# Performance work log

Hardware: AMD Instinct MI355X
Metric: run time of the kernel (lower is better)

The kernel has to match this reference:

```python
import jax, jax.numpy as jnp
import numpy as np

B, S, H, K = 8, 2048, 768, 128
FILTERS = (1, 3, 5)
C = H // len(FILTERS)  # 256 channels per conv, concat -> H
LN_EPS = 1e-05
COS_EPS = 1e-08


def setup_inputs() -> dict:
    key = jax.random.key(0)
    ks = jax.random.split(key, 16)
    mk = lambda k, shape: jax.random.normal(k, shape, dtype=jnp.float32) * 0.02
    return {
        "representation": jax.random.normal(ks[0], (B, S, H), dtype=jnp.float32),
        "src_mask": jnp.ones((B, S), dtype=jnp.float32),
        # conv weights stored as [k, H_in, C_out] for lax 1D conv (torch Conv2d(1,C,(k,H)))
        "enc_conv_w1": mk(ks[1], (1, H, C)),
        "enc_conv_w3": mk(ks[2], (3, H, C)),
        "enc_conv_w5": mk(ks[3], (5, H, C)),
        "ln_g": jnp.ones((H,), jnp.float32),
        "ln_b": jnp.zeros((H,), jnp.float32),
        "enc_lin_w": mk(ks[4], (H, H)),   # torch Linear weight [out,in]
        "enc_tr_w": mk(ks[5], (K, H)),
        "dec_tr_w": mk(ks[6], (H, K)),
        "dec_conv_w1": mk(ks[7], (1, H, C)),
        "dec_conv_w3": mk(ks[8], (3, H, C)),
        "dec_conv_w5": mk(ks[9], (5, H, C)),
        "dec_lin_w": mk(ks[10], (H, H)),
        "out_lin_w": mk(ks[11], (H, H)),
    }


def _multi_conv(x, ws):
    # x: [B, S, H]; each w: [k, H, C]; torch pads (k//2, 0) -> same-length for odd k
    outs = []
    for w in ws:
        k = w.shape[0]
        outs.append(jax.lax.conv_general_dilated(
            x, w, window_strides=(1,), padding=[(k // 2, k // 2)],
            dimension_numbers=("NWC", "WIO", "NWC")))
    return jnp.concatenate(outs, axis=-1)  # [B, S, H]


def _layernorm(x, g, b):
    mu = jnp.mean(x, axis=-1, keepdims=True)
    var = jnp.mean((x - mu) ** 2, axis=-1, keepdims=True)
    return (x - mu) * jax.lax.rsqrt(var + LN_EPS) * g + b


def reference(representation, src_mask, enc_conv_w1, enc_conv_w3, enc_conv_w5,
              ln_g, ln_b, enc_lin_w, enc_tr_w, dec_tr_w,
              dec_conv_w1, dec_conv_w3, dec_conv_w5, dec_lin_w, out_lin_w):
    # ---- AutoEncoder (dropout layers are identity in eval mode) ----
    h = _multi_conv(representation, (enc_conv_w1, enc_conv_w3, enc_conv_w5))
    h = _layernorm(h + representation, ln_g, ln_b)
    h = jnp.tanh(h @ enc_lin_w.T)
    location = h @ enc_tr_w.T            # [B, S, K] (encode_out)
    d = location @ dec_tr_w.T            # [B, S, H]
    d = _multi_conv(d, (dec_conv_w1, dec_conv_w3, dec_conv_w5))
    d = jnp.tanh(d @ dec_lin_w.T)
    decode_out = d @ out_lin_w.T         # [B, S, H]

    # ---- banded pairwise cosine similarity (fuses the torch shift loop) ----
    # torch loop writes dis_matrix[b, i, i+s+1] = cos(loc[b, i+s+1], loc[b, i])
    # for s in range(max_act_len), i.e. the strict upper band of the symmetric
    # pairwise cosine-similarity matrix with offsets 1..max_act_len.
    normed = location / jnp.maximum(
        jnp.sqrt(jnp.sum(location * location, axis=-1, keepdims=True)), COS_EPS)
    sim = jnp.einsum("bid,bjd->bij", normed, normed)  # [B, S, S]
    offs = jnp.arange(S)[None, :] - jnp.arange(S)[:, None]  # j - i
    max_act_len = jnp.max(jnp.sum(src_mask, axis=-1)).astype(jnp.int32)
    band = (offs >= 1) & (offs <= max_act_len)        # [S, S]
    dis_matrix = jnp.where(band[None], sim, 0.0)
    src_dis_mask = src_mask[:, :, None] * src_mask[:, None, :]
    act_dis_tags = band[None].astype(jnp.float32) * src_dis_mask
    return (location, dis_matrix, act_dis_tags, decode_out)
```

## Files before the change

### kernel.cpp

```cpp
#include <hip/hip_runtime.h>

#define B_   8
#define S_   2048
#define H_   768
#define K_   128
#define C_   256
#define SH_  2052
#define MTOK (B_*S_)

typedef __attribute__((ext_vector_type(8))) short short8;
typedef __attribute__((ext_vector_type(4))) float f32x4;

typedef __attribute__((address_space(1))) const void gvoid;
typedef __attribute__((address_space(3))) void lvoid;

__device__ __forceinline__ void gload16(const void* g, void* l) {
    __builtin_amdgcn_global_load_lds((gvoid*)g, (lvoid*)l, 16, 0, 0);
}

__device__ __forceinline__ ushort f2b(float f) {
    union { float f; unsigned u; } v; v.f = f;
    unsigned r = v.u + 0x7fffu + ((v.u >> 16) & 1u);
    return (ushort)(r >> 16);
}
__device__ __forceinline__ float b2f(ushort u) {
    union { unsigned u; float f; } v; v.u = ((unsigned)u) << 16;
    return v.f;
}
__device__ __forceinline__ float fast_tanh(float x) {
    float e = __expf(2.f * x);
    return 1.f - 2.f / (e + 1.f);
}


__global__ __launch_bounds__(512) void k_maxlen(const float* __restrict__ mask, int* Lp) {
    __shared__ float sh[8];
    const int tid = threadIdx.x;
    float mx = 0.f;
    for (int b = 0; b < B_; ++b) {
        const float4 v = ((const float4*)(mask + b * S_))[tid];
        float s = v.x + v.y + v.z + v.w;
#pragma unroll
        for (int off = 32; off; off >>= 1) s += __shfl_xor(s, off);
        if ((tid & 63) == 0) sh[tid >> 6] = s;
        __syncthreads();
        if (tid == 0) {
            float t = 0.f;
#pragma unroll
            for (int q = 0; q < 8; ++q) t += sh[q];
            mx = fmaxf(mx, t);
        }
        __syncthreads();
    }
    if (tid == 0) *Lp = (int)mx;
}

__global__ void k_build_xh(const float* __restrict__ rep, ushort* __restrict__ xh) {
    int i = blockIdx.x * blockDim.x + threadIdx.x;
    const int stride = gridDim.x * blockDim.x;
    const int n4 = B_ * SH_ * H_ / 4;
    for (; i < n4; i += stride) {
        const int idx = i * 4;
        const int h = idx % H_;
        const int rs = idx / H_;
        const int s = rs % SH_;
        const int b = rs / SH_;
        ushort4 o; o.x = 0; o.y = 0; o.z = 0; o.w = 0;
        if (s >= 2 && s < S_ + 2) {
            const float4 v = *(const float4*)(rep + ((size_t)b * S_ + (s - 2)) * H_ + h);
            o.x = f2b(v.x); o.y = f2b(v.y); o.z = f2b(v.z); o.w = f2b(v.w);
        }
        *(ushort4*)(xh + idx) = o;
    }
}

struct CvtE { const float* src; ushort* dst; int n; int kh; };
struct CvtAll { CvtE e[11]; };

__global__ void k_cvt_all(CvtAll a) {
    const CvtE e = a.e[blockIdx.y];
    int i = blockIdx.x * blockDim.x + threadIdx.x;
    const int stride = gridDim.x * blockDim.x;
    for (; i < e.n; i += stride) {
        if (e.kh) {
            const int c = i / e.kh;
            const int r = i - c * e.kh;
            e.dst[i] = f2b(e.src[r * C_ + c]);
        } else {
            e.dst[i] = f2b(e.src[i]);
        }
    }
}


struct G3P {
    const ushort* A;
    const ushort* W0;
    const ushort* W1;
    const ushort* W2;
    int lda;
    ushort* outB; int ldoB;
    int nMtiles;
};

__global__ __launch_bounds__(512, 2) void g3(G3P p) {
    constexpr int ASEG = 1024;
    constexpr int BSEG = 2048;
    constexpr int BUFE = (ASEG + BSEG) * 8;
    __shared__ __align__(16) ushort lds[3][BUFE];

    const int tid = threadIdx.x;
    const int w = tid >> 6, lane = tid & 63;
    const int l15 = lane & 15, lk = lane >> 4;
    const int wr = w >> 2, wc = w & 3;
    const int axor = l15 & 7;

    const int nM = p.nMtiles;
    int idx = blockIdx.x;
    int br;
    if (idx < nM) br = 2;
    else if (idx < 2 * nM) { br = 1; idx -= nM; }
    else { br = 0; idx -= 2 * nM; }
    const int m_base = idx * 128;
    const int n_base = br * 256;
    const int nt = 12 * (2 * br + 1);
    const int Ktot = 768 * (2 * br + 1);
    const ushort* Wt = (br == 0) ? p.W0 : (br == 1) ? p.W1 : p.W2;
    const int arow0 = m_base + ((m_base >> 11) << 2) + (2 - br);

    auto stage1 = [&](int kt, int bufi, int q) {
        const int kk = kt << 6;
        const int tap = kt / 12;
        const int h0 = (kt - tap * 12) << 6;
        if (q < 2) {
            const int seg = q * 512 + tid;
            const int row = seg >> 3;
            const int slot = (seg & 7) ^ (row & 7);
            gload16(p.A + (size_t)(arow0 + tap + row) * p.lda + h0 + slot * 8,
                    &lds[bufi][seg * 8]);
        } else {
            const int seg = (q - 2) * 512 + tid;
            const int row = seg >> 3;
            const int slot = (seg & 7) ^ (row & 7);
            gload16(Wt + (size_t)row * Ktot + kk + slot * 8,
                    &lds[bufi][ASEG * 8 + seg * 8]);
        }
    };
    auto stage = [&](int kt, int bufi) {
#pragma unroll
        for (int q = 0; q < 6; ++q) stage1(kt, bufi, q);
    };

    f32x4 acc[4][4] = {};

    stage(0, 0);
    stage(1, 1);

    int buf = 0;
    for (int t = 0; t < nt; ++t) {
        const ushort* Ab = &lds[buf][0];
        const ushort* Bb = &lds[buf][ASEG * 8];
        if (t + 1 < nt) asm volatile("s_waitcnt vmcnt(6)" ::: "memory");
        else            asm volatile("s_waitcnt vmcnt(0)" ::: "memory");
        __builtin_amdgcn_sched_barrier(0);
        asm volatile("s_barrier" ::: "memory");
        __builtin_amdgcn_sched_barrier(0);

        int nbuf = buf + 2; if (nbuf >= 3) nbuf -= 3;
        const bool sb = (t + 2 < nt);

#pragma unroll
        for (int ks = 0; ks < 2; ++ks) {
            short8 bq[4], aq[4];
#pragma unroll
            for (int ni = 0; ni < 4; ++ni)
                bq[ni] = *(const short8*)(Bb + (wc * 64 + ni * 16 + l15) * 64 + ((((ks << 2) | lk) ^ axor) << 3));
#pragma unroll
            for (int mi = 0; mi < 4; ++mi)
                aq[mi] = *(const short8*)(Ab + (wr * 64 + mi * 16 + l15) * 64 + ((((ks << 2) | lk) ^ axor) << 3));
            if (sb) { stage1(t + 2, nbuf, 3 * ks); stage1(t + 2, nbuf, 3 * ks + 1); stage1(t + 2, nbuf, 3 * ks + 2); }
            asm volatile("s_waitcnt lgkmcnt(0)" ::: "memory");
            __builtin_amdgcn_sched_barrier(0);
            __builtin_amdgcn_s_setprio(1);
#pragma unroll
            for (int mi = 0; mi < 4; ++mi)
#pragma unroll
                for (int ni = 0; ni < 4; ++ni)
                    acc[mi][ni] = __builtin_amdgcn_mfma_f32_16x16x32_bf16(aq[mi], bq[ni], acc[mi][ni], 0, 0, 0);
            __builtin_amdgcn_s_setprio(0);
            __builtin_amdgcn_sched_barrier(0);
        }
        ++buf; if (buf == 3) buf = 0;
    }

#pragma unroll
    for (int mi = 0; mi < 4; ++mi)
#pragma unroll
        for (int ni = 0; ni < 4; ++ni)
#pragma unroll
            for (int jj = 0; jj < 4; ++jj) {
                const int r = m_base + wr * 64 + mi * 16 + 4 * lk + jj;
                const int n = n_base + wc * 64 + ni * 16 + l15;
                p.outB[(size_t)r * p.ldoB + n] = f2b(acc[mi][ni][jj]);
            }
}


struct G4P {
    const ushort* A;
    const ushort* W;
    int Ktot;
    int lda;
    ushort* outB; int ldoB;
    float*  outF; int ldoF;
    int act;
};

__global__ __launch_bounds__(256, 2) void g4(G4P p) {
    constexpr int ASEG = 1024;
    constexpr int BSEG = 1536;
    __shared__ __align__(16) ushort lds[2][(ASEG + BSEG) * 8];

    const int tid = threadIdx.x;
    const int w = tid >> 6, lane = tid & 63;
    const int l15 = lane & 15, lk = lane >> 4;
    const int wr = w >> 1, wc = w & 1;
    const int axor = l15 & 7;
    const int m_base = blockIdx.x * 128;
    const int n_base = blockIdx.y * 192;
    const int nt = p.Ktot >> 6;

    auto stage = [&](int kt, int bufi) {
        const int kk = kt << 6;
        ushort* Ab = &lds[bufi][0];
        ushort* Bb = &lds[bufi][ASEG * 8];
#pragma unroll
        for (int q = 0; q < 4; ++q) {
            const int seg = q * 256 + tid;
            const int row = seg >> 3;
            const int s = (seg & 7) ^ (row & 7);
            gload16(p.A + (size_t)(m_base + row) * p.lda + kk + s * 8, Ab + seg * 8);
        }
#pragma unroll
        for (int q = 0; q < 6; ++q) {
            const int seg = q * 256 + tid;
            const int row = seg >> 3;
            const int s = (seg & 7) ^ (row & 7);
            gload16(p.W + (size_t)(n_base + row) * p.Ktot + kk + s * 8, Bb + seg * 8);
        }
    };

    f32x4 acc[4][6] = {};

    stage(0, 0);
    stage(1, 1);

    for (int t = 0; t < nt; ++t) {
        const int cur = t & 1;
        const ushort* Ab = &lds[cur][0];
        const ushort* Bb = &lds[cur][ASEG * 8];
        if (t + 1 < nt) asm volatile("s_waitcnt vmcnt(10)" ::: "memory");
        else            asm volatile("s_waitcnt vmcnt(0)" ::: "memory");
        __builtin_amdgcn_sched_barrier(0);
        asm volatile("s_barrier" ::: "memory");
        __builtin_amdgcn_sched_barrier(0);

        short8 af[4][2], bf[6][2];
#pragma unroll
        for (int mi = 0; mi < 4; ++mi)
#pragma unroll
            for (int ks = 0; ks < 2; ++ks)
                af[mi][ks] = *(const short8*)(Ab + (wr * 64 + mi * 16 + l15) * 64 + ((((ks << 2) | lk) ^ axor) << 3));
#pragma unroll
        for (int ni = 0; ni < 6; ++ni)
#pragma unroll
            for (int ks = 0; ks < 2; ++ks)
                bf[ni][ks] = *(const short8*)(Bb + (wc * 96 + ni * 16 + l15) * 64 + ((((ks << 2) | lk) ^ axor) << 3));
        asm volatile("s_waitcnt lgkmcnt(0)" ::: "memory");
        __builtin_amdgcn_sched_barrier(0);
        asm volatile("s_barrier" ::: "memory");
        __builtin_amdgcn_sched_barrier(0);
        if (t + 2 < nt) stage(t + 2, cur);
        __builtin_amdgcn_sched_barrier(0);
        __builtin_amdgcn_s_setprio(1);
#pragma unroll
        for (int mi = 0; mi < 4; ++mi)
#pragma unroll
            for (int ni = 0; ni < 6; ++ni) {
                acc[mi][ni] = __builtin_amdgcn_mfma_f32_16x16x32_bf16(af[mi][0], bf[ni][0], acc[mi][ni], 0, 0, 0);
                acc[mi][ni] = __builtin_amdgcn_mfma_f32_16x16x32_bf16(af[mi][1], bf[ni][1], acc[mi][ni], 0, 0, 0);
            }
        __builtin_amdgcn_s_setprio(0);
        __builtin_amdgcn_sched_barrier(0);
    }

#pragma unroll
    for (int mi = 0; mi < 4; ++mi)
#pragma unroll
        for (int ni = 0; ni < 6; ++ni)
#pragma unroll
            for (int jj = 0; jj < 4; ++jj) {
                const int r = m_base + wr * 64 + mi * 16 + 4 * lk + jj;
                const int n = n_base + wc * 96 + ni * 16 + l15;
                float v = acc[mi][ni][jj];
                if (p.act) v = fast_tanh(v);
                if (p.outF) p.outF[(size_t)r * p.ldoF + n] = v;
                if (p.outB) p.outB[(size_t)r * p.ldoB + n] = f2b(v);
            }
}


struct GemmP {
    const ushort* A;
    const ushort* Wt;
    int Ktot;
    int lda;
    ushort* outB;
    int ldoB;
    int outB_halo;
    float* outF;
    int ldoF;
    int act;
};

template<int BM, int BN>
__global__ __launch_bounds__(256) void gemm_lds(GemmP p) {
    constexpr int MF = BM / 32;
    constexpr int NF = BN / 32;
    __shared__ __align__(16) ushort As[BM * 64];
    __shared__ __align__(16) ushort Bs[BN * 64];
    const int tid = threadIdx.x;
    const int w = tid >> 6, lane = tid & 63;
    const int l15 = lane & 15, lk = lane >> 4;
    const int m_base = blockIdx.x * BM;
    const int n_base = blockIdx.y * BN;
    const int wr = w >> 1, wc = w & 1;
    f32x4 acc[MF][NF] = {};
    const int srow = lane >> 3;
    const int scol = (lane & 7) * 8;
    const int nk = p.Ktot >> 6;

    for (int kt = 0; kt < nk; ++kt) {
        const int kk = kt << 6;
#pragma unroll
        for (int q = 0; q < BM / 32; ++q) {
            const int r = w * (BM / 4) + q * 8;
            gload16(p.A + (size_t)(m_base + r + srow) * p.lda + kk + scol, As + r * 64);
        }
#pragma unroll
        for (int q = 0; q < BN / 32; ++q) {
            const int r = w * (BN / 4) + q * 8;
            gload16(p.Wt + (size_t)(n_base + r + srow) * p.Ktot + kk + scol, Bs + r * 64);
        }
        __syncthreads();
#pragma unroll
        for (int ks = 0; ks < 2; ++ks) {
            short8 af[MF], bfr[NF];
#pragma unroll
            for (int i = 0; i < MF; ++i)
                af[i] = *(const short8*)(As + (wr * (BM / 2) + i * 16 + l15) * 64 + ks * 32 + 8 * lk);
#pragma unroll
            for (int j = 0; j < NF; ++j)
                bfr[j] = *(const short8*)(Bs + (wc * (BN / 2) + j * 16 + l15) * 64 + ks * 32 + 8 * lk);
#pragma unroll
            for (int i = 0; i < MF; ++i)
#pragma unroll
                for (int j = 0; j < NF; ++j)
                    acc[i][j] = __builtin_amdgcn_mfma_f32_16x16x32_bf16(af[i], bfr[j], acc[i][j], 0, 0, 0);
        }
        __syncthreads();
    }

    const int bb4 = ((m_base >> 11) << 2) + 2;
#pragma unroll
    for (int i = 0; i < MF; ++i)
#pragma unroll
        for (int j = 0; j < NF; ++j)
#pragma unroll
            for (int jj = 0; jj < 4; ++jj) {
                const int r = m_base + wr * (BM / 2) + i * 16 + 4 * lk + jj;
                const int n = n_base + wc * (BN / 2) + j * 16 + l15;
                float v = acc[i][j][jj];
                if (p.act) v = fast_tanh(v);
                if (p.outF) p.outF[(size_t)r * p.ldoF + n] = v;
                if (p.outB) {
                    const int rr = p.outB_halo ? (r + bb4) : r;
                    p.outB[(size_t)rr * p.ldoB + n] = f2b(v);
                }
            }
}


__global__ __launch_bounds__(192) void k_ln(const ushort* __restrict__ conv,
                                            const float* __restrict__ rep,
                                            const float* __restrict__ gw,
                                            const float* __restrict__ bw,
                                            ushort* __restrict__ out) {
    const int row = blockIdx.x;
    const int tid = threadIdx.x;
    const int h = tid * 4;
    const ushort4 cv = *(const ushort4*)(conv + (size_t)row * H_ + h);
    const float4  rv = *(const float4*)(rep + (size_t)row * H_ + h);
    float v[4] = { b2f(cv.x) + rv.x, b2f(cv.y) + rv.y, b2f(cv.z) + rv.z, b2f(cv.w) + rv.w };
    float s1 = v[0] + v[1] + v[2] + v[3];
    float s2 = v[0]*v[0] + v[1]*v[1] + v[2]*v[2] + v[3]*v[3];
#pragma unroll
    for (int off = 32; off; off >>= 1) { s1 += __shfl_xor(s1, off); s2 += __shfl_xor(s2, off); }
    __shared__ float sh[6];
    const int wid = tid >> 6, lane = tid & 63;
    if (lane == 0) { sh[wid] = s1; sh[3 + wid] = s2; }
    __syncthreads();
    s1 = sh[0] + sh[1] + sh[2];
    s2 = sh[3] + sh[4] + sh[5];
    const float mu  = s1 * (1.f / H_);
    const float var = s2 * (1.f / H_) - mu * mu;
    const float rs  = rsqrtf(var + 1e-5f);
    const float4 gv = *(const float4*)(gw + h);
    const float4 bv = *(const float4*)(bw + h);
    ushort4 o;
    o.x = f2b((v[0] - mu) * rs * gv.x + bv.x);
    o.y = f2b((v[1] - mu) * rs * gv.y + bv.y);
    o.z = f2b((v[2] - mu) * rs * gv.z + bv.z);
    o.w = f2b((v[3] - mu) * rs * gv.w + bv.w);
    *(ushort4*)(out + (size_t)row * H_ + h) = o;
}


__global__ __launch_bounds__(256) void k_normed(const float* __restrict__ loc, ushort* __restrict__ out) {
    const int wid = threadIdx.x >> 6, lane = threadIdx.x & 63;
    const int row = blockIdx.x * 4 + wid;
    const float* lp = loc + (size_t)row * K_;
    const float x0 = lp[lane], x1 = lp[lane + 64];
    float ss = x0 * x0 + x1 * x1;
#pragma unroll
    for (int off = 32; off; off >>= 1) ss += __shfl_xor(ss, off);
    const float sc = 1.f / fmaxf(sqrtf(ss), 1e-8f);
    ushort* op = out + (size_t)row * K_;
    op[lane] = f2b(x0 * sc);
    op[lane + 64] = f2b(x1 * sc);
}


__global__ __launch_bounds__(256) void k_simtags(const ushort* __restrict__ normed,
                                                 const float* __restrict__ mask,
                                                 const int* __restrict__ Lp,
                                                 float* __restrict__ dis,
                                                 float* __restrict__ tags) {
    const int wid = threadIdx.x >> 6, lane = threadIdx.x & 63;
    const int l15 = lane & 15, lk = lane >> 4;
    const int b   = blockIdx.z;
    const int i0b = blockIdx.x * 64;
    const int i0  = i0b + wid * 16;
    const int j0  = blockIdx.y * 64;
    const int L   = *Lp;
    f32x4 acc[4] = {};
    if ((j0 + 63 >= i0b + 1) && (j0 <= i0b + 63 + L)) {
        const ushort* nb = normed + (size_t)b * S_ * K_;
#pragma unroll
        for (int kt = 0; kt < 4; ++kt) {
            const int kk = kt * 32;
            const short8 a = *(const short8*)(nb + (size_t)(i0 + l15) * K_ + kk + 8 * lk);
#pragma unroll
            for (int j = 0; j < 4; ++j) {
                const short8 bfr = *(const short8*)(nb + (size_t)(j0 + j * 16 + l15) * K_ + kk + 8 * lk);
                acc[j] = __builtin_amdgcn_mfma_f32_16x16x32_bf16(a, bfr, acc[j], 0, 0, 0);
            }
        }
    }
    const float* mb = mask + b * S_;
    float* dp = dis  + (size_t)b * S_ * S_;
    float* tp = tags + (size_t)b * S_ * S_;
#pragma unroll
    for (int j = 0; j < 4; ++j) {
#pragma unroll
        for (int jj = 0; jj < 4; ++jj) {
            const int i  = i0 + 4 * lk + jj;
            const int jc = j0 + j * 16 + l15;
            const int d  = jc - i;
            const bool band = (d >= 1 && d <= L);
            dp[(size_t)i * S_ + jc] = band ? acc[j][jj] : 0.f;
            tp[(size_t)i * S_ + jc] = band ? mb[i] * mb[jc] : 0.f;
        }
    }
}


extern "C" void kernel_launch(void* const* d_in, const int* in_sizes, int n_in,
                              void* d_out, int out_size, void* d_ws, size_t ws_size,
                              hipStream_t stream) {
    const float* rep  = (const float*)d_in[0];
    const float* mask = (const float*)d_in[1];
    const float* ew1  = (const float*)d_in[2];
    const float* ew3  = (const float*)d_in[3];
    const float* ew5  = (const float*)d_in[4];
    const float* lng  = (const float*)d_in[5];
    const float* lnb  = (const float*)d_in[6];
    const float* elin = (const float*)d_in[7];
    const float* etr  = (const float*)d_in[8];
    const float* dtr  = (const float*)d_in[9];
    const float* dw1  = (const float*)d_in[10];
    const float* dw3  = (const float*)d_in[11];
    const float* dw5  = (const float*)d_in[12];
    const float* dlin = (const float*)d_in[13];
    const float* olin = (const float*)d_in[14];

    float* out_loc = (float*)d_out;
    float* out_dis = out_loc + (size_t)B_ * S_ * K_;
    float* out_tag = out_dis + (size_t)B_ * S_ * S_;
    float* out_dec = out_tag + (size_t)B_ * S_ * S_;

    char* ws = (char*)d_ws;
    size_t off = 0;
    auto alloc = [&](size_t bytes) -> char* {
        char* p = ws + off;
        off += (bytes + 255) & ~(size_t)255;
        return p;
    };
    int*    Lp    = (int*)alloc(256);
    ushort* Xh    = (ushort*)alloc((size_t)B_ * SH_ * H_ * 2);
    ushort* wte1  = (ushort*)alloc((size_t)C_ * 768 * 2);
    ushort* wte3  = (ushort*)alloc((size_t)C_ * 2304 * 2);
    ushort* wte5  = (ushort*)alloc((size_t)C_ * 3840 * 2);
    ushort* wtd1  = (ushort*)alloc((size_t)C_ * 768 * 2);
    ushort* wtd3  = (ushort*)alloc((size_t)C_ * 2304 * 2);
    ushort* wtd5  = (ushort*)alloc((size_t)C_ * 3840 * 2);
    ushort* welin = (ushort*)alloc((size_t)H_ * H_ * 2);
    ushort* wetr  = (ushort*)alloc((size_t)K_ * H_ * 2);
    ushort* wdtr  = (ushort*)alloc((size_t)H_ * K_ * 2);
    ushort* wdlin = (ushort*)alloc((size_t)H_ * H_ * 2);
    ushort* wolin = (ushort*)alloc((size_t)H_ * H_ * 2);
    ushort* bufB  = (ushort*)alloc((size_t)MTOK * H_ * 2);
    ushort* bufC  = (ushort*)alloc((size_t)MTOK * H_ * 2);
    ushort* bufD  = (ushort*)alloc((size_t)MTOK * H_ * 2);
    ushort* bufL  = (ushort*)alloc((size_t)MTOK * K_ * 2);
    ushort* bufN  = (ushort*)alloc((size_t)MTOK * K_ * 2);
    if (ws_size < off) return;

    k_maxlen<<<1, 512, 0, stream>>>(mask, Lp);
    k_build_xh<<<2048, 256, 0, stream>>>(rep, Xh);

    CvtAll ca;
    ca.e[0]  = { ew1,  wte1, 768 * C_,  768 };
    ca.e[1]  = { ew3,  wte3, 2304 * C_, 2304 };
    ca.e[2]  = { ew5,  wte5, 3840 * C_, 3840 };
    ca.e[3]  = { dw1,  wtd1, 768 * C_,  768 };
    ca.e[4]  = { dw3,  wtd3, 2304 * C_, 2304 };
    ca.e[5]  = { dw5,  wtd5, 3840 * C_, 3840 };
    ca.e[6]  = { elin, welin, H_ * H_, 0 };
    ca.e[7]  = { etr,  wetr,  K_ * H_, 0 };
    ca.e[8]  = { dtr,  wdtr,  H_ * K_, 0 };
    ca.e[9]  = { dlin, wdlin, H_ * H_, 0 };
    ca.e[10] = { olin, wolin, H_ * H_, 0 };
    k_cvt_all<<<dim3(256, 11), 256, 0, stream>>>(ca);

    {
        G3P p{}; p.A = Xh; p.W0 = wte1; p.W1 = wte3; p.W2 = wte5;
        p.lda = H_; p.outB = bufB; p.ldoB = H_; p.nMtiles = MTOK / 128;
        g3<<<3 * (MTOK / 128), 512, 0, stream>>>(p);
    }
    k_ln<<<MTOK, 192, 0, stream>>>(bufB, rep, lng, lnb, bufC);
    {
        G4P p{}; p.A = bufC; p.W = welin; p.Ktot = H_; p.lda = H_;
        p.outB = bufD; p.ldoB = H_; p.act = 1;
        g4<<<dim3(MTOK / 128, H_ / 192), 256, 0, stream>>>(p);
    }
    {
        GemmP p{}; p.A = bufD; p.lda = H_; p.Wt = wetr; p.Ktot = H_;
        p.outF = out_loc; p.ldoF = K_; p.outB = bufL; p.ldoB = K_;
        gemm_lds<64, 128><<<dim3(MTOK / 64, 1), 256, 0, stream>>>(p);
    }
    k_normed<<<MTOK / 4, 256, 0, stream>>>(out_loc, bufN);
    {
        GemmP p{}; p.A = bufL; p.lda = K_; p.Wt = wdtr; p.Ktot = K_;
        p.outB = Xh; p.ldoB = H_; p.outB_halo = 1;
        gemm_lds<128, 128><<<dim3(MTOK / 128, H_ / 128), 256, 0, stream>>>(p);
    }
    {
        G3P p{}; p.A = Xh; p.W0 = wtd1; p.W1 = wtd3; p.W2 = wtd5;
        p.lda = H_; p.outB = bufB; p.ldoB = H_; p.nMtiles = MTOK / 128;
        g3<<<3 * (MTOK / 128), 512, 0, stream>>>(p);
    }
    {
        G4P p{}; p.A = bufB; p.W = wdlin; p.Ktot = H_; p.lda = H_;
        p.outB = bufC; p.ldoB = H_; p.act = 1;
        g4<<<dim3(MTOK / 128, H_ / 192), 256, 0, stream>>>(p);
    }
    {
        G4P p{}; p.A = bufC; p.W = wolin; p.Ktot = H_; p.lda = H_;
        p.outF = out_dec; p.ldoF = H_;
        g4<<<dim3(MTOK / 128, H_ / 192), 256, 0, stream>>>(p);
    }
    k_simtags<<<dim3(S_ / 64, S_ / 64, B_), 256, 0, stream>>>(bufN, mask, Lp, out_dis, out_tag);
}
```

Baseline: 429.2 us.

## Fold decoder transform weight into decoder conv weights to shrink conv K dimension

Precomputes composite weights (dec_tr_w folded into each decoder conv tap) with a small MFMA kernel, so the decoder conv runs directly on the 128-wide location tensor instead of the 768-wide decoded tensor. This removes the separate location→H GEMM and its 768-wide intermediate write, and cuts the decoder conv's reduction depth sixfold. Location is now written into a halo-padded buffer whose halo rows are zeroed in the maxlen kernel. The trade-off is an extra bf16 rounding of the composed weights, which changes numerics slightly.

```diff
diff --git a/kernel.cpp b/kernel.cpp
--- a/kernel.cpp
+++ b/kernel.cpp
@@ -33,7 +33,8 @@
 }
 
 
-__global__ __launch_bounds__(512) void k_maxlen(const float* __restrict__ mask, int* Lp) {
+__global__ __launch_bounds__(512) void k_maxlen(const float* __restrict__ mask, int* Lp,
+                                                ushort* __restrict__ lh) {
     __shared__ float sh[8];
     const int tid = threadIdx.x;
     float mx = 0.f;
@@ -53,6 +54,14 @@
         __syncthreads();
     }
     if (tid == 0) *Lp = (int)mx;
+    for (int i = tid; i < B_ * 4 * K_; i += 512) {
+        const int b = i >> 9;
+        const int rc = i & 511;
+        const int rr = rc >> 7;
+        const int cc = rc & 127;
+        const int row = (rr < 2) ? rr : (2048 + rr);
+        lh[((size_t)b * SH_ + row) * K_ + cc] = 0;
+    }
 }
 
 __global__ void k_build_xh(const float* __restrict__ rep, ushort* __restrict__ xh) {
@@ -74,7 +83,7 @@
     }
 }
 
-struct CvtE { const float* src; ushort* dst; int n; int kh; };
+struct CvtE { const float* src; ushort* dst; int n; int kh; int sld; };
 struct CvtAll { CvtE e[11]; };
 
 __global__ void k_cvt_all(CvtAll a) {
@@ -85,11 +94,66 @@
         if (e.kh) {
             const int c = i / e.kh;
             const int r = i - c * e.kh;
-            e.dst[i] = f2b(e.src[r * C_ + c]);
+            e.dst[i] = f2b(e.src[r * e.sld + c]);
         } else {
             e.dst[i] = f2b(e.src[i]);
         }
     }
+}
+
+
+struct CompE { const ushort* w; int wld; int woff; ushort* o; int old_; int koff; };
+struct CompP { const ushort* dtrT; CompE e[9]; };
+
+__global__ __launch_bounds__(256) void k_compw(CompP p) {
+    __shared__ __align__(16) ushort As[128 * 64];
+    __shared__ __align__(16) ushort Bs[128 * 64];
+    const CompE e = p.e[blockIdx.y];
+    const int tid = threadIdx.x;
+    const int w = tid >> 6, lane = tid & 63;
+    const int l15 = lane & 15, lk = lane >> 4;
+    const int wr = w >> 1, wc = w & 1;
+    const int n_base = blockIdx.x * 128;
+    f32x4 acc[4][4] = {};
+    const int srow = lane >> 3;
+    const int scol = (lane & 7) * 8;
+
+    for (int kt = 0; kt < 12; ++kt) {
+        const int kk = kt << 6;
+#pragma unroll
+        for (int q = 0; q < 4; ++q) {
+            const int r = w * 32 + q * 8;
+            gload16(p.dtrT + (size_t)(r + srow) * 768 + kk + scol, As + r * 64);
+            gload16(e.w + (size_t)(n_base + r + srow) * e.wld + e.woff + kk + scol, Bs + r * 64);
+        }
+        __syncthreads();
+#pragma unroll
+        for (int ks = 0; ks < 2; ++ks) {
+            short8 af[4], bfr[4];
+#pragma unroll
+            for (int i = 0; i < 4; ++i)
+                af[i] = *(const short8*)(As + (wr * 64 + i * 16 + l15) * 64 + ks * 32 + 8 * lk);
+#pragma unroll
+            for (int j = 0; j < 4; ++j)
+                bfr[j] = *(const short8*)(Bs + (wc * 64 + j * 16 + l15) * 64 + ks * 32 + 8 * lk);
+#pragma unroll
+            for (int i = 0; i < 4; ++i)
+#pragma unroll
+                for (int j = 0; j < 4; ++j)
+                    acc[i][j] = __builtin_amdgcn_mfma_f32_16x16x32_bf16(af[i], bfr[j], acc[i][j], 0, 0, 0);
+        }
+        __syncthreads();
+    }
+#pragma unroll
+    for (int i = 0; i < 4; ++i)
+#pragma unroll
+        for (int j = 0; j < 4; ++j)
+#pragma unroll
+            for (int jj = 0; jj < 4; ++jj) {
+                const int jr = wr * 64 + i * 16 + 4 * lk + jj;
+                const int c  = n_base + wc * 64 + j * 16 + l15;
+                e.o[(size_t)c * e.old_ + e.koff + jr] = f2b(acc[i][j][jj]);
+            }
 }
 
 
@@ -103,7 +167,10 @@
     int nMtiles;
 };
 
+template<bool DEC>
 __global__ __launch_bounds__(512, 2) void g3(G3P p) {
+    constexpr int TPT = DEC ? 2 : 12;
+    constexpr int LDA = DEC ? 128 : 768;
     constexpr int ASEG = 1024;
     constexpr int BSEG = 2048;
     constexpr int BUFE = (ASEG + BSEG) * 8;
@@ -123,26 +190,25 @@
     else { br = 0; idx -= 2 * nM; }
     const int m_base = idx * 128;
     const int n_base = br * 256;
-    const int nt = 12 * (2 * br + 1);
-    const int Ktot = 768 * (2 * br + 1);
+    const int nt = TPT * (2 * br + 1);
+    const int Ktot = LDA * (2 * br + 1);
     const ushort* Wt = (br == 0) ? p.W0 : (br == 1) ? p.W1 : p.W2;
     const int arow0 = m_base + ((m_base >> 11) << 2) + (2 - br);
 
     auto stage1 = [&](int kt, int bufi, int q) {
-        const int kk = kt << 6;
-        const int tap = kt / 12;
-        const int h0 = (kt - tap * 12) << 6;
+        const int tap = kt / TPT;
+        const int h0 = (kt - tap * TPT) << 6;
         if (q < 2) {
             const int seg = q * 512 + tid;
             const int row = seg >> 3;
             const int slot = (seg & 7) ^ (row & 7);
-            gload16(p.A + (size_t)(arow0 + tap + row) * p.lda + h0 + slot * 8,
+            gload16(p.A + (size_t)(arow0 + tap + row) * LDA + h0 + slot * 8,
                     &lds[bufi][seg * 8]);
         } else {
             const int seg = (q - 2) * 512 + tid;
             const int row = seg >> 3;
             const int slot = (seg & 7) ^ (row & 7);
-            gload16(Wt + (size_t)row * Ktot + kk + slot * 8,
+            gload16(Wt + (size_t)row * Ktot + (kt << 6) + slot * 8,
                     &lds[bufi][ASEG * 8 + seg * 8]);
         }
     };
@@ -518,6 +584,7 @@
     };
     int*    Lp    = (int*)alloc(256);
     ushort* Xh    = (ushort*)alloc((size_t)B_ * SH_ * H_ * 2);
+    ushort* bufLh = (ushort*)alloc((size_t)B_ * SH_ * K_ * 2);
     ushort* wte1  = (ushort*)alloc((size_t)C_ * 768 * 2);
     ushort* wte3  = (ushort*)alloc((size_t)C_ * 2304 * 2);
     ushort* wte5  = (ushort*)alloc((size_t)C_ * 3840 * 2);
@@ -526,37 +593,47 @@
     ushort* wtd5  = (ushort*)alloc((size_t)C_ * 3840 * 2);
     ushort* welin = (ushort*)alloc((size_t)H_ * H_ * 2);
     ushort* wetr  = (ushort*)alloc((size_t)K_ * H_ * 2);
-    ushort* wdtr  = (ushort*)alloc((size_t)H_ * K_ * 2);
+    ushort* dtrT  = (ushort*)alloc((size_t)K_ * H_ * 2);
     ushort* wdlin = (ushort*)alloc((size_t)H_ * H_ * 2);
     ushort* wolin = (ushort*)alloc((size_t)H_ * H_ * 2);
+    ushort* wc1   = (ushort*)alloc((size_t)C_ * 128 * 2);
+    ushort* wc3   = (ushort*)alloc((size_t)C_ * 384 * 2);
+    ushort* wc5   = (ushort*)alloc((size_t)C_ * 640 * 2);
     ushort* bufB  = (ushort*)alloc((size_t)MTOK * H_ * 2);
     ushort* bufC  = (ushort*)alloc((size_t)MTOK * H_ * 2);
     ushort* bufD  = (ushort*)alloc((size_t)MTOK * H_ * 2);
-    ushort* bufL  = (ushort*)alloc((size_t)MTOK * K_ * 2);
     ushort* bufN  = (ushort*)alloc((size_t)MTOK * K_ * 2);
     if (ws_size < off) return;
 
-    k_maxlen<<<1, 512, 0, stream>>>(mask, Lp);
+    k_maxlen<<<1, 512, 0, stream>>>(mask, Lp, bufLh);
     k_build_xh<<<2048, 256, 0, stream>>>(rep, Xh);
 
     CvtAll ca;
-    ca.e[0]  = { ew1,  wte1, 768 * C_,  768 };
-    ca.e[1]  = { ew3,  wte3, 2304 * C_, 2304 };
-    ca.e[2]  = { ew5,  wte5, 3840 * C_, 3840 };
-    ca.e[3]  = { dw1,  wtd1, 768 * C_,  768 };
-    ca.e[4]  = { dw3,  wtd3, 2304 * C_, 2304 };
-    ca.e[5]  = { dw5,  wtd5, 3840 * C_, 3840 };
-    ca.e[6]  = { elin, welin, H_ * H_, 0 };
-    ca.e[7]  = { etr,  wetr,  K_ * H_, 0 };
-    ca.e[8]  = { dtr,  wdtr,  H_ * K_, 0 };
-    ca.e[9]  = { dlin, wdlin, H_ * H_, 0 };
-    ca.e[10] = { olin, wolin, H_ * H_, 0 };
+    ca.e[0]  = { ew1,  wte1, 768 * C_,  768,  C_ };
+    ca.e[1]  = { ew3,  wte3, 2304 * C_, 2304, C_ };
+    ca.e[2]  = { ew5,  wte5, 3840 * C_, 3840, C_ };
+    ca.e[3]  = { dw1,  wtd1, 768 * C_,  768,  C_ };
+    ca.e[4]  = { dw3,  wtd3, 2304 * C_, 2304, C_ };
+    ca.e[5]  = { dw5,  wtd5, 3840 * C_, 3840, C_ };
+    ca.e[6]  = { elin, welin, H_ * H_, 0, 0 };
+    ca.e[7]  = { etr,  wetr,  K_ * H_, 0, 0 };
+    ca.e[8]  = { dlin, wdlin, H_ * H_, 0, 0 };
+    ca.e[9]  = { olin, wolin, H_ * H_, 0, 0 };
+    ca.e[10] = { dtr,  dtrT,  K_ * H_, 768, K_ };
     k_cvt_all<<<dim3(256, 11), 256, 0, stream>>>(ca);
+
+    {
+        CompP cp; cp.dtrT = dtrT;
+        cp.e[0] = { wtd1, 768,  0,        wc1, 128, 0 };
+        for (int t = 0; t < 3; ++t) cp.e[1 + t] = { wtd3, 2304, t * 768, wc3, 384, t * 128 };
+        for (int t = 0; t < 5; ++t) cp.e[4 + t] = { wtd5, 3840, t * 768, wc5, 640, t * 128 };
+        k_compw<<<dim3(2, 9), 256, 0, stream>>>(cp);
+    }
 
     {
         G3P p{}; p.A = Xh; p.W0 = wte1; p.W1 = wte3; p.W2 = wte5;
         p.lda = H_; p.outB = bufB; p.ldoB = H_; p.nMtiles = MTOK / 128;
-        g3<<<3 * (MTOK / 128), 512, 0, stream>>>(p);
+        g3<false><<<3 * (MTOK / 128), 512, 0, stream>>>(p);
     }
     k_ln<<<MTOK, 192, 0, stream>>>(bufB, rep, lng, lnb, bufC);
     {
@@ -566,19 +643,14 @@
     }
     {
         GemmP p{}; p.A = bufD; p.lda = H_; p.Wt = wetr; p.Ktot = H_;
-        p.outF = out_loc; p.ldoF = K_; p.outB = bufL; p.ldoB = K_;
+        p.outF = out_loc; p.ldoF = K_; p.outB = bufLh; p.ldoB = K_; p.outB_halo = 1;
         gemm_lds<64, 128><<<dim3(MTOK / 64, 1), 256, 0, stream>>>(p);
     }
     k_normed<<<MTOK / 4, 256, 0, stream>>>(out_loc, bufN);
     {
-        GemmP p{}; p.A = bufL; p.lda = K_; p.Wt = wdtr; p.Ktot = K_;
-        p.outB = Xh; p.ldoB = H_; p.outB_halo = 1;
-        gemm_lds<128, 128><<<dim3(MTOK / 128, H_ / 128), 256, 0, stream>>>(p);
-    }
-    {
-        G3P p{}; p.A = Xh; p.W0 = wtd1; p.W1 = wtd3; p.W2 = wtd5;
-        p.lda = H_; p.outB = bufB; p.ldoB = H_; p.nMtiles = MTOK / 128;
-        g3<<<3 * (MTOK / 128), 512, 0, stream>>>(p);
+        G3P p{}; p.A = bufLh; p.W0 = wc1; p.W1 = wc3; p.W2 = wc5;
+        p.lda = K_; p.outB = bufB; p.ldoB = H_; p.nMtiles = MTOK / 128;
+        g3<true><<<3 * (MTOK / 128), 512, 0, stream>>>(p);
     }
     {
         G4P p{}; p.A = bufB; p.W = wdlin; p.Ktot = H_; p.lda = H_;
```

After: 386.9 us. 9.9% less time.
